# Performance work log

Hardware: AMD Instinct MI355X
Metric: run time of the kernel (lower is better)

## Reference

```python
import jax, jax.numpy as jnp
import numpy as np

N_NODES = 100000
N_EDGES = 1600000
D_IN = 64
D_HID = 64
NEG_SLOPE = 0.01  # torch leaky_relu default


def _sage_conv(x, src, dst, W_l, b_l, W_r):
    # PyG SAGEConv (mean aggr): lin_l(mean_j x_j) + lin_r(x_i)
    n = x.shape[0]
    msg = x[src]  # [E, D] irregular gather
    agg = jax.ops.segment_sum(msg, dst, num_segments=n)
    deg = jax.ops.segment_sum(jnp.ones((src.shape[0],), x.dtype), dst, num_segments=n)
    mean = agg / jnp.maximum(deg, 1.0)[:, None]
    return mean @ W_l.T + b_l + x @ W_r.T


def setup_inputs() -> dict:
    key = jax.random.key(0)
    ks = jax.random.split(key, 12)
    x = jax.random.normal(ks[0], (N_NODES, D_IN), dtype=jnp.float32)
    edge_index = jax.random.randint(ks[1], (2, N_EDGES), 0, N_NODES, dtype=jnp.int64)
    s = 1.0 / np.sqrt(D_IN)
    params = {}
    dims = [(D_IN, D_HID), (D_HID, D_HID), (D_HID, D_HID)]
    ki = 2
    for i, (din, dout) in enumerate(dims, start=1):
        sc = 1.0 / np.sqrt(din)
        params[f'W_l{i}'] = jax.random.uniform(ks[ki], (dout, din), minval=-sc, maxval=sc, dtype=jnp.float32); ki += 1
        params[f'b_l{i}'] = jnp.zeros((dout,), jnp.float32)
        params[f'W_r{i}'] = jax.random.uniform(ks[ki], (dout, din), minval=-sc, maxval=sc, dtype=jnp.float32); ki += 1
    sc = 1.0 / np.sqrt(D_HID)
    params['W_out'] = jax.random.uniform(ks[ki], (1, D_HID), minval=-sc, maxval=sc, dtype=jnp.float32)
    params['b_out'] = jnp.zeros((1,), jnp.float32)
    return {'x': x, 'edge_index': edge_index, **params}


def reference(x, edge_index, W_l1, b_l1, W_r1, W_l2, b_l2, W_r2, W_l3, b_l3, W_r3, W_out, b_out):
    src, dst = edge_index[0], edge_index[1]
    h = x
    for (Wl, bl, Wr) in ((W_l1, b_l1, W_r1), (W_l2, b_l2, W_r2), (W_l3, b_l3, W_r3)):
        h = _sage_conv(h, src, dst, Wl, bl, Wr)
        h = jnp.where(h >= 0, h, NEG_SLOPE * h)
        # dropout is identity in eval mode
    return h @ W_out.T + b_out  # [N, 1]
```

## Files before the change

### kernel.cpp

```cpp
#include <hip/hip_runtime.h>
#include <hip/hip_fp16.h>

#define D 64
#define NEG_SLOPE 0.01f
#define CB_SHIFT 9
#define CB_NODES 512
#define MAXCB 256
#define CHUNK 8192
#define BCAP 10240
#define SADJ_CAP 10240
#define SA_STRIDE 132
#define SW_STRIDE 68

struct GemmSmem {
    float sA[64 * SA_STRIDE];
    float sW[64 * SW_STRIDE];
};
struct ScatSmem {
    int hist[MAXCB];
    int lofs[MAXCB];
    int gbase[MAXCB];
    int cur[MAXCB];
    int swsum[4];
    unsigned spk[CHUNK];
    unsigned char sbk[CHUNK];
};
union FusedSmem { GemmSmem g; ScatSmem s; };

__device__ __forceinline__ int detect64(const void* __restrict__ ei) {
    int lane = threadIdx.x & 63;
    int v = ((const int*)ei)[2 * lane + 1];
    return (__ballot(v != 0) == 0ULL) ? 1 : 0;
}

__device__ __forceinline__ int edge_at(const void* __restrict__ ei, long long idx, int is64) {
    if (is64) return (int)((const long long*)ei)[idx];
    return ((const int*)ei)[idx];
}

__device__ __forceinline__ void scatter_body(ScatSmem& sm,
        const void* __restrict__ ei, long long E,
        int* __restrict__ bcursor, unsigned* __restrict__ ebuf,
        int ncb, int bid) {
    int t = threadIdx.x;
    sm.hist[t] = 0;
    int is64 = detect64(ei);
    __syncthreads();
    long long start = (long long)bid * CHUNK;
    int ccnt = (int)min((long long)CHUNK, E - start);

    for (int i = t; i < ccnt; i += 256) {
        int d = edge_at(ei, E + start + i, is64);
        atomicAdd(&sm.hist[d >> CB_SHIFT], 1);
    }
    __syncthreads();
    {
        int v = sm.hist[t];
        int lane = t & 63, w = t >> 6;
        int inc = v;
        for (int off = 1; off < 64; off <<= 1) {
            int u = __shfl_up(inc, off, 64);
            if (lane >= off) inc += u;
        }
        if (lane == 63) sm.swsum[w] = inc;
        __syncthreads();
        int wof = 0;
        for (int i = 0; i < w; ++i) wof += sm.swsum[i];
        sm.lofs[t] = wof + inc - v;
    }
    if (t < ncb && sm.hist[t]) sm.gbase[t] = atomicAdd(&bcursor[t], sm.hist[t]);
    __syncthreads();
    sm.cur[t] = sm.lofs[t];
    __syncthreads();

    for (int i = t; i < ccnt; i += 256) {
        int s = edge_at(ei, start + i, is64);
        int d = edge_at(ei, E + start + i, is64);
        int b = d >> CB_SHIFT;
        int slot = atomicAdd(&sm.cur[b], 1);
        sm.spk[slot] = ((unsigned)s << CB_SHIFT) | (unsigned)(d & (CB_NODES - 1));
        sm.sbk[slot] = (unsigned char)b;
    }
    __syncthreads();

    for (int i = t; i < ccnt; i += 256) {
        int b = sm.sbk[i];
        int dst = sm.gbase[b] + (i - sm.lofs[b]);
        if (dst < BCAP) ebuf[(size_t)b * BCAP + dst] = sm.spk[i];
    }
}

__device__ __forceinline__ void stage_tile_T(float* __restrict__ sA,
        const float* __restrict__ g, int node_base, int N, int t) {
    int nq = t >> 4;
    int kq = t & 15;
#pragma unroll
    for (int p = 0; p < 8; ++p) {
        int node = p * 16 + nq;
        int gn = node_base + node;
        if (gn >= N) gn = N - 1;
        const float4 v = *(const float4*)(g + (size_t)gn * D + (kq << 2));
        sA[(kq * 4 + 0) * SA_STRIDE + node] = v.x;
        sA[(kq * 4 + 1) * SA_STRIDE + node] = v.y;
        sA[(kq * 4 + 2) * SA_STRIDE + node] = v.z;
        sA[(kq * 4 + 3) * SA_STRIDE + node] = v.w;
    }
}

__device__ __forceinline__ void stage_w_T(float* __restrict__ sW,
        const float* __restrict__ W, int t) {
    int cq = t >> 4;
    int kq = t & 15;
#pragma unroll
    for (int p = 0; p < 4; ++p) {
        int c = p * 16 + cq;
        const float4 v = *(const float4*)(W + c * D + (kq << 2));
        sW[(kq * 4 + 0) * SW_STRIDE + c] = v.x;
        sW[(kq * 4 + 1) * SW_STRIDE + c] = v.y;
        sW[(kq * 4 + 2) * SW_STRIDE + c] = v.z;
        sW[(kq * 4 + 3) * SW_STRIDE + c] = v.w;
    }
}

__device__ __forceinline__ void kloop4(float acc[8][4],
        const float* __restrict__ sA, const float* __restrict__ sW,
        int ng, int cg) {
#pragma unroll 4
    for (int k = 0; k < 64; ++k) {
        const float4 qa0 = *(const float4*)&sA[k * SA_STRIDE + ng * 8];
        const float4 qa1 = *(const float4*)&sA[k * SA_STRIDE + ng * 8 + 4];
        const float4 qb  = *(const float4*)&sW[k * SW_STRIDE + cg * 4];
        float av[8] = {qa0.x, qa0.y, qa0.z, qa0.w, qa1.x, qa1.y, qa1.z, qa1.w};
        float bv[4] = {qb.x, qb.y, qb.z, qb.w};
#pragma unroll
        for (int i = 0; i < 8; ++i)
#pragma unroll
            for (int j = 0; j < 4; ++j)
                acc[i][j] = __builtin_fmaf(av[i], bv[j], acc[i][j]);
    }
}

__device__ __forceinline__ void gemm_body(GemmSmem& sm,
        const float* __restrict__ h, const float* __restrict__ Wl,
        const float* __restrict__ Wr, const float* __restrict__ bl,
        __half* __restrict__ P, float* __restrict__ R, int N, int bid) {
    int t = threadIdx.x;
    int node_base = bid * 128;

    stage_tile_T(sm.sA, h, node_base, N, t);
    stage_w_T(sm.sW, Wl, t);
    __syncthreads();

    int ng = t >> 4;
    int cg = t & 15;
    float accP[8][4], accR[8][4];
#pragma unroll
    for (int i = 0; i < 8; ++i)
#pragma unroll
        for (int j = 0; j < 4; ++j) { accP[i][j] = 0.f; accR[i][j] = 0.f; }

    kloop4(accP, sm.sA, sm.sW, ng, cg);
    __syncthreads();
    stage_w_T(sm.sW, Wr, t);
    __syncthreads();
    kloop4(accR, sm.sA, sm.sW, ng, cg);

    const float4 bq = *(const float4*)&bl[cg * 4];
#pragma unroll
    for (int i = 0; i < 8; ++i) {
        int gn = node_base + ng * 8 + i;
        if (gn < N) {
            __half2* ph = (__half2*)(P + (size_t)gn * D + cg * 4);
            ph[0] = __floats2half2_rn(accP[i][0], accP[i][1]);
            ph[1] = __floats2half2_rn(accP[i][2], accP[i][3]);
            *(float4*)(R + (size_t)gn * D + cg * 4) =
                make_float4(accR[i][0] + bq.x, accR[i][1] + bq.y,
                            accR[i][2] + bq.z, accR[i][3] + bq.w);
        }
    }
}

__global__ __launch_bounds__(256, 3) void gemm1_scatter_kernel(
        const void* __restrict__ ei, long long E,
        int* __restrict__ bcursor, unsigned* __restrict__ ebuf, int ncb, int sgrid,
        const float* __restrict__ h, const float* __restrict__ Wl,
        const float* __restrict__ Wr, const float* __restrict__ bl,
        __half* __restrict__ P, float* __restrict__ R, int N) {
    __shared__ FusedSmem sm;
    if ((int)blockIdx.x < sgrid) {
        scatter_body(sm.s, ei, E, bcursor, ebuf, ncb, blockIdx.x);
    } else {
        gemm_body(sm.g, h, Wl, Wr, bl, P, R, N, blockIdx.x - sgrid);
    }
}

__global__ __launch_bounds__(256, 3) void gemm_kernel(
        const float* __restrict__ h, const float* __restrict__ Wl,
        const float* __restrict__ Wr, const float* __restrict__ bl,
        __half* __restrict__ P, float* __restrict__ R, int N) {
    __shared__ GemmSmem sm;
    gemm_body(sm, h, Wl, Wr, bl, P, R, N, blockIdx.x);
}

__global__ __launch_bounds__(256) void finefill_kernel(
        const unsigned* __restrict__ ebuf, const int* __restrict__ bcount,
        int* __restrict__ rowptr, int* __restrict__ adj, int N, int ncb) {
    __shared__ int cnt[CB_NODES];
    __shared__ int cur[CB_NODES];
    __shared__ int wpart[4];
    __shared__ int wsum4[4];
    __shared__ int se0;
    __shared__ int sAdj[SADJ_CAP];
    int t = threadIdx.x;
    int b = blockIdx.x;

    {
        int v = (t < ncb) ? min(bcount[t], BCAP) : 0;
        int lane = t & 63, w = t >> 6;
        int inc = v;
        for (int off = 1; off < 64; off <<= 1) {
            int u = __shfl_up(inc, off, 64);
            if (lane >= off) inc += u;
        }
        if (lane == 63) wsum4[w] = inc;
        __syncthreads();
        int wof = 0;
        for (int iw = 0; iw < w; ++iw) wof += wsum4[iw];
        int ex = wof + inc - v;
        if (t == b) se0 = ex;
        if (b == 0 && t == 0)
            rowptr[N] = wsum4[0] + wsum4[1] + wsum4[2] + wsum4[3];
    }
    __syncthreads();
    int e0 = se0;
    int len = min(bcount[b], BCAP);
    int nb = b << CB_SHIFT;
    const unsigned* slab = ebuf + (size_t)b * BCAP;

    cnt[2 * t] = 0; cnt[2 * t + 1] = 0;
    __syncthreads();
    for (int i = t; i < len; i += 256) {
        unsigned p = slab[i];
        atomicAdd(&cnt[p & (CB_NODES - 1)], 1);
    }
    __syncthreads();

    int c0 = cnt[2 * t], c1 = cnt[2 * t + 1];
    int s = c0 + c1;
    int lane = t & 63, wv = t >> 6;
    int inc = s;
    for (int off = 1; off < 64; off <<= 1) {
        int u = __shfl_up(inc, off, 64);
        if (lane >= off) inc += u;
    }
    if (lane == 63) wpart[wv] = inc;
    __syncthreads();
    int wof = 0;
    for (int w = 0; w < wv; ++w) wof += wpart[w];
    int ex = wof + inc - s;
    cur[2 * t] = ex; cur[2 * t + 1] = ex + c0;
    {
        int g = nb + 2 * t;
        if (g < N)     rowptr[g]     = e0 + ex;
        if (g + 1 < N) rowptr[g + 1] = e0 + ex + c0;
    }
    __syncthreads();

    int big = (len > SADJ_CAP);
    for (int i = t; i < len; i += 256) {
        unsigned p = slab[i];
        int dl = (int)(p & (CB_NODES - 1));
        int src = (int)(p >> CB_SHIFT);
        int pos = atomicAdd(&cur[dl], 1);
        if (big) adj[e0 + pos] = src;
        else     sAdj[pos] = src;
    }
    __syncthreads();
    if (!big) {
        for (int i = t; i < len; i += 256) adj[e0 + i] = sAdj[i];
    }
}

__global__ __launch_bounds__(256) void agg3_kernel(
        const __half* __restrict__ P, const float* __restrict__ R,
        const int* __restrict__ rowptr, const int* __restrict__ adj,
        const float* __restrict__ Wout, const float* __restrict__ bout,
        float* __restrict__ hout, float* __restrict__ out,
        int N, int final_flag) {
    int tid = blockIdx.x * blockDim.x + threadIdx.x;
    int i = tid >> 3;
    int sub = tid & 7;
    if (i >= N) return;

    int b0 = rowptr[i], b1 = rowptr[i + 1];
    float a0 = 0.f, a1 = 0.f, a2 = 0.f, a3 = 0.f;
    float a4 = 0.f, a5 = 0.f, a6 = 0.f, a7 = 0.f;
    size_t cofs = (size_t)(sub << 3);

    int e = b0;
    int nfull = (b1 - b0) >> 2;
#pragma unroll 2
    for (int q = 0; q < nfull; ++q) {
        int s0 = adj[e], s1 = adj[e + 1], s2 = adj[e + 2], s3 = adj[e + 3];
        e += 4;
        union { float4 f4; __half2 h2[4]; } u0, u1, u2, u3;
        u0.f4 = *(const float4*)(P + (size_t)s0 * D + cofs);
        u1.f4 = *(const float4*)(P + (size_t)s1 * D + cofs);
        u2.f4 = *(const float4*)(P + (size_t)s2 * D + cofs);
        u3.f4 = *(const float4*)(P + (size_t)s3 * D + cofs);
#define ACC8(u) { \
        float2 v0 = __half22float2(u.h2[0]); float2 v1 = __half22float2(u.h2[1]); \
        float2 v2 = __half22float2(u.h2[2]); float2 v3 = __half22float2(u.h2[3]); \
        a0 += v0.x; a1 += v0.y; a2 += v1.x; a3 += v1.y; \
        a4 += v2.x; a5 += v2.y; a6 += v3.x; a7 += v3.y; }
        ACC8(u0) ACC8(u1) ACC8(u2) ACC8(u3)
    }
    for (; e < b1; ++e) {
        int s = adj[e];
        union { float4 f4; __half2 h2[4]; } u;
        u.f4 = *(const float4*)(P + (size_t)s * D + cofs);
        ACC8(u)
    }
#undef ACC8

    float inv = 1.0f / fmaxf((float)(b1 - b0), 1.0f);
    const float4 r0 = *(const float4*)(R + (size_t)i * D + cofs);
    const float4 r1 = *(const float4*)(R + (size_t)i * D + cofs + 4);
    float y0 = a0 * inv + r0.x; y0 = (y0 >= 0.f) ? y0 : NEG_SLOPE * y0;
    float y1 = a1 * inv + r0.y; y1 = (y1 >= 0.f) ? y1 : NEG_SLOPE * y1;
    float y2 = a2 * inv + r0.z; y2 = (y2 >= 0.f) ? y2 : NEG_SLOPE * y2;
    float y3 = a3 * inv + r0.w; y3 = (y3 >= 0.f) ? y3 : NEG_SLOPE * y3;
    float y4 = a4 * inv + r1.x; y4 = (y4 >= 0.f) ? y4 : NEG_SLOPE * y4;
    float y5 = a5 * inv + r1.y; y5 = (y5 >= 0.f) ? y5 : NEG_SLOPE * y5;
    float y6 = a6 * inv + r1.z; y6 = (y6 >= 0.f) ? y6 : NEG_SLOPE * y6;
    float y7 = a7 * inv + r1.w; y7 = (y7 >= 0.f) ? y7 : NEG_SLOPE * y7;
    if (!final_flag) {
        *(float4*)(hout + (size_t)i * D + cofs) = make_float4(y0, y1, y2, y3);
        *(float4*)(hout + (size_t)i * D + cofs + 4) = make_float4(y4, y5, y6, y7);
    } else {
        const float4 w0 = *(const float4*)(Wout + cofs);
        const float4 w1 = *(const float4*)(Wout + cofs + 4);
        float p = y0 * w0.x + y1 * w0.y + y2 * w0.z + y3 * w0.w
                + y4 * w1.x + y5 * w1.y + y6 * w1.z + y7 * w1.w;
        p += __shfl_xor(p, 1, 64);
        p += __shfl_xor(p, 2, 64);
        p += __shfl_xor(p, 4, 64);
        if (sub == 0) out[i] = p + bout[0];
    }
}

extern "C" void kernel_launch(void* const* d_in, const int* in_sizes, int n_in,
                              void* d_out, int out_size, void* d_ws, size_t ws_size,
                              hipStream_t stream) {
    const float* x    = (const float*)d_in[0];
    const void*  ei   = d_in[1];
    const float* Wl1  = (const float*)d_in[2];
    const float* bl1  = (const float*)d_in[3];
    const float* Wr1  = (const float*)d_in[4];
    const float* Wl2  = (const float*)d_in[5];
    const float* bl2  = (const float*)d_in[6];
    const float* Wr2  = (const float*)d_in[7];
    const float* Wl3  = (const float*)d_in[8];
    const float* bl3  = (const float*)d_in[9];
    const float* Wr3  = (const float*)d_in[10];
    const float* Wout = (const float*)d_in[11];
    const float* bout = (const float*)d_in[12];
    float* out = (float*)d_out;

    int       N = in_sizes[0] / D;
    long long E = (long long)in_sizes[1] / 2;
    int ncb = (N + CB_NODES - 1) >> CB_SHIFT;

    char* ws = (char*)d_ws;
    size_t off = 256;
    int* bcursor = (int*)(ws + off); off += 1024;
    int* rowptr = (int*)(ws + off); off += (((size_t)(N + 1) * 4 + 255) / 256) * 256;
    int* adj    = (int*)(ws + off); off += (((size_t)E * 4 + 255) / 256) * 256;
    unsigned* ebuf = (unsigned*)(ws + off); off += (size_t)ncb * BCAP * 4;
    float* B1 = (float*)(ws + off); off += (size_t)N * D * 4;
    __half* B2h = (__half*)(ws + off);

    int sgrid = (int)((E + CHUNK - 1) / CHUNK);
    int ggrid = (N + 127) / 128;
    int agrid = (N * 8 + 255) / 256;

    hipMemsetAsync(bcursor, 0, 1024, stream);

    gemm1_scatter_kernel<<<sgrid + ggrid, 256, 0, stream>>>(
        ei, E, bcursor, ebuf, ncb, sgrid,
        x, Wl1, Wr1, bl1, B2h, B1, N);
    finefill_kernel<<<ncb, 256, 0, stream>>>(ebuf, bcursor, rowptr, adj, N, ncb);
    agg3_kernel<<<agrid, 256, 0, stream>>>(B2h, B1, rowptr, adj, Wout, bout, B1, out, N, 0);
    gemm_kernel<<<ggrid, 256, 0, stream>>>(B1, Wl2, Wr2, bl2, B2h, B1, N);
    agg3_kernel<<<agrid, 256, 0, stream>>>(B2h, B1, rowptr, adj, Wout, bout, B1, out, N, 0);
    gemm_kernel<<<ggrid, 256, 0, stream>>>(B1, Wl3, Wr3, bl3, B2h, B1, N);
    agg3_kernel<<<agrid, 256, 0, stream>>>(B2h, B1, rowptr, adj, Wout, bout, B1, out, N, 1);
}
```

Measured before the change: 314.0 us.

## Replace FP32 FMA GEMM with FP16 MFMA 16x16x32 matrix cores

The per-layer dense transform (h@Wl and h@Wr) is rewritten to convert the node tile and both weight matrices to fp16 in shared memory, then compute with MFMA 16x16x32 f16 instructions instead of scalar FMA loops. Both weight matrices are staged at once, which drops a barrier and the restaging pass. Shared memory shrinks, so launch bounds go up to 4 blocks per CU and the scatter CHUNK is halved to fit the union. Feeding fp16 inputs to the R path adds rounding error, and the output stores become scalar and strided.

```diff
diff --git a/kernel.cpp b/kernel.cpp
--- a/kernel.cpp
+++ b/kernel.cpp
@@ -6,15 +6,18 @@
 #define CB_SHIFT 9
 #define CB_NODES 512
 #define MAXCB 256
-#define CHUNK 8192
+#define CHUNK 4096
 #define BCAP 10240
 #define SADJ_CAP 10240
-#define SA_STRIDE 132
-#define SW_STRIDE 68
+#define SAH 72
+
+typedef _Float16 f16x8 __attribute__((ext_vector_type(8)));
+typedef _Float16 f16x4 __attribute__((ext_vector_type(4)));
+typedef float    f32x4 __attribute__((ext_vector_type(4)));
 
 struct GemmSmem {
-    float sA[64 * SA_STRIDE];
-    float sW[64 * SW_STRIDE];
+    _Float16 sA[128 * SAH];
+    _Float16 sW[2 * 64 * SAH];
 };
 struct ScatSmem {
     int hist[MAXCB];
@@ -90,56 +93,6 @@
     }
 }
 
-__device__ __forceinline__ void stage_tile_T(float* __restrict__ sA,
-        const float* __restrict__ g, int node_base, int N, int t) {
-    int nq = t >> 4;
-    int kq = t & 15;
-#pragma unroll
-    for (int p = 0; p < 8; ++p) {
-        int node = p * 16 + nq;
-        int gn = node_base + node;
-        if (gn >= N) gn = N - 1;
-        const float4 v = *(const float4*)(g + (size_t)gn * D + (kq << 2));
-        sA[(kq * 4 + 0) * SA_STRIDE + node] = v.x;
-        sA[(kq * 4 + 1) * SA_STRIDE + node] = v.y;
-        sA[(kq * 4 + 2) * SA_STRIDE + node] = v.z;
-        sA[(kq * 4 + 3) * SA_STRIDE + node] = v.w;
-    }
-}
-
-__device__ __forceinline__ void stage_w_T(float* __restrict__ sW,
-        const float* __restrict__ W, int t) {
-    int cq = t >> 4;
-    int kq = t & 15;
-#pragma unroll
-    for (int p = 0; p < 4; ++p) {
-        int c = p * 16 + cq;
-        const float4 v = *(const float4*)(W + c * D + (kq << 2));
-        sW[(kq * 4 + 0) * SW_STRIDE + c] = v.x;
-        sW[(kq * 4 + 1) * SW_STRIDE + c] = v.y;
-        sW[(kq * 4 + 2) * SW_STRIDE + c] = v.z;
-        sW[(kq * 4 + 3) * SW_STRIDE + c] = v.w;
-    }
-}
-
-__device__ __forceinline__ void kloop4(float acc[8][4],
-        const float* __restrict__ sA, const float* __restrict__ sW,
-        int ng, int cg) {
-#pragma unroll 4
-    for (int k = 0; k < 64; ++k) {
-        const float4 qa0 = *(const float4*)&sA[k * SA_STRIDE + ng * 8];
-        const float4 qa1 = *(const float4*)&sA[k * SA_STRIDE + ng * 8 + 4];
-        const float4 qb  = *(const float4*)&sW[k * SW_STRIDE + cg * 4];
-        float av[8] = {qa0.x, qa0.y, qa0.z, qa0.w, qa1.x, qa1.y, qa1.z, qa1.w};
-        float bv[4] = {qb.x, qb.y, qb.z, qb.w};
-#pragma unroll
-        for (int i = 0; i < 8; ++i)
-#pragma unroll
-            for (int j = 0; j < 4; ++j)
-                acc[i][j] = __builtin_fmaf(av[i], bv[j], acc[i][j]);
-    }
-}
-
 __device__ __forceinline__ void gemm_body(GemmSmem& sm,
         const float* __restrict__ h, const float* __restrict__ Wl,
         const float* __restrict__ Wr, const float* __restrict__ bl,
@@ -147,40 +100,91 @@
     int t = threadIdx.x;
     int node_base = bid * 128;
 
-    stage_tile_T(sm.sA, h, node_base, N, t);
-    stage_w_T(sm.sW, Wl, t);
-    __syncthreads();
-
-    int ng = t >> 4;
-    int cg = t & 15;
-    float accP[8][4], accR[8][4];
-#pragma unroll
-    for (int i = 0; i < 8; ++i)
-#pragma unroll
-        for (int j = 0; j < 4; ++j) { accP[i][j] = 0.f; accR[i][j] = 0.f; }
-
-    kloop4(accP, sm.sA, sm.sW, ng, cg);
-    __syncthreads();
-    stage_w_T(sm.sW, Wr, t);
-    __syncthreads();
-    kloop4(accR, sm.sA, sm.sW, ng, cg);
-
-    const float4 bq = *(const float4*)&bl[cg * 4];
-#pragma unroll
-    for (int i = 0; i < 8; ++i) {
-        int gn = node_base + ng * 8 + i;
-        if (gn < N) {
-            __half2* ph = (__half2*)(P + (size_t)gn * D + cg * 4);
-            ph[0] = __floats2half2_rn(accP[i][0], accP[i][1]);
-            ph[1] = __floats2half2_rn(accP[i][2], accP[i][3]);
-            *(float4*)(R + (size_t)gn * D + cg * 4) =
-                make_float4(accR[i][0] + bq.x, accR[i][1] + bq.y,
-                            accR[i][2] + bq.z, accR[i][3] + bq.w);
-        }
-    }
-}
-
-__global__ __launch_bounds__(256, 3) void gemm1_scatter_kernel(
+    {
+        int r = t >> 1, j = t & 1;
+        int gn = node_base + r; if (gn >= N) gn = N - 1;
+        const float* src = h + (size_t)gn * D + j * 32;
+        _Float16* dst = sm.sA + r * SAH + j * 32;
+#pragma unroll
+        for (int q = 0; q < 8; ++q) {
+            const float4 v = *(const float4*)(src + q * 4);
+            f16x4 o = { (_Float16)v.x, (_Float16)v.y, (_Float16)v.z, (_Float16)v.w };
+            *(f16x4*)(dst + q * 4) = o;
+        }
+    }
+    {
+        const float* W = (t < 128) ? Wl : Wr;
+        int tt = t & 127;
+        int r = tt >> 1, j = tt & 1;
+        const float* src = W + r * D + j * 32;
+        _Float16* dst = sm.sW + ((t < 128) ? 0 : 64 * SAH) + r * SAH + j * 32;
+#pragma unroll
+        for (int q = 0; q < 8; ++q) {
+            const float4 v = *(const float4*)(src + q * 4);
+            f16x4 o = { (_Float16)v.x, (_Float16)v.y, (_Float16)v.z, (_Float16)v.w };
+            *(f16x4*)(dst + q * 4) = o;
+        }
+    }
+    __syncthreads();
+
+    int w = t >> 6, lane = t & 63;
+    int lr = lane & 15;
+    int lk = lane >> 4;
+
+    f16x8 af[2][2];
+#pragma unroll
+    for (int mt = 0; mt < 2; ++mt)
+#pragma unroll
+        for (int ks = 0; ks < 2; ++ks)
+            af[mt][ks] = *(const f16x8*)(sm.sA
+                + (w * 32 + mt * 16 + lr) * SAH + ks * 32 + lk * 8);
+
+    f32x4 accP[2][4], accR[2][4];
+#pragma unroll
+    for (int mt = 0; mt < 2; ++mt)
+#pragma unroll
+        for (int nt = 0; nt < 4; ++nt) {
+            accP[mt][nt] = (f32x4){0.f, 0.f, 0.f, 0.f};
+            accR[mt][nt] = (f32x4){0.f, 0.f, 0.f, 0.f};
+        }
+
+#pragma unroll
+    for (int nt = 0; nt < 4; ++nt) {
+        const _Float16* wrow = sm.sW + (nt * 16 + lr) * SAH + lk * 8;
+        f16x8 b0 = *(const f16x8*)(wrow);
+        f16x8 b1 = *(const f16x8*)(wrow + 32);
+        f16x8 c0 = *(const f16x8*)(wrow + 64 * SAH);
+        f16x8 c1 = *(const f16x8*)(wrow + 64 * SAH + 32);
+        accP[0][nt] = __builtin_amdgcn_mfma_f32_16x16x32_f16(af[0][0], b0, accP[0][nt], 0, 0, 0);
+        accP[0][nt] = __builtin_amdgcn_mfma_f32_16x16x32_f16(af[0][1], b1, accP[0][nt], 0, 0, 0);
+        accP[1][nt] = __builtin_amdgcn_mfma_f32_16x16x32_f16(af[1][0], b0, accP[1][nt], 0, 0, 0);
+        accP[1][nt] = __builtin_amdgcn_mfma_f32_16x16x32_f16(af[1][1], b1, accP[1][nt], 0, 0, 0);
+        accR[0][nt] = __builtin_amdgcn_mfma_f32_16x16x32_f16(af[0][0], c0, accR[0][nt], 0, 0, 0);
+        accR[0][nt] = __builtin_amdgcn_mfma_f32_16x16x32_f16(af[0][1], c1, accR[0][nt], 0, 0, 0);
+        accR[1][nt] = __builtin_amdgcn_mfma_f32_16x16x32_f16(af[1][0], c0, accR[1][nt], 0, 0, 0);
+        accR[1][nt] = __builtin_amdgcn_mfma_f32_16x16x32_f16(af[1][1], c1, accR[1][nt], 0, 0, 0);
+    }
+
+#pragma unroll
+    for (int nt = 0; nt < 4; ++nt) {
+        int ch = nt * 16 + lr;
+        float bv = bl[ch];
+#pragma unroll
+        for (int mt = 0; mt < 2; ++mt) {
+            int nrow = node_base + w * 32 + mt * 16 + lk * 4;
+#pragma unroll
+            for (int r = 0; r < 4; ++r) {
+                int gn = nrow + r;
+                if (gn < N) {
+                    P[(size_t)gn * D + ch] = __float2half(accP[mt][nt][r]);
+                    R[(size_t)gn * D + ch] = accR[mt][nt][r] + bv;
+                }
+            }
+        }
+    }
+}
+
+__global__ __launch_bounds__(256, 4) void gemm1_scatter_kernel(
         const void* __restrict__ ei, long long E,
         int* __restrict__ bcursor, unsigned* __restrict__ ebuf, int ncb, int sgrid,
         const float* __restrict__ h, const float* __restrict__ Wl,
@@ -194,7 +198,7 @@
     }
 }
 
-__global__ __launch_bounds__(256, 3) void gemm_kernel(
+__global__ __launch_bounds__(256, 4) void gemm_kernel(
         const float* __restrict__ h, const float* __restrict__ Wl,
         const float* __restrict__ Wr, const float* __restrict__ bl,
         __half* __restrict__ P, float* __restrict__ R, int N) {
```

Result: faster. 281.9 us (-10.2%).
